# Kernel optimization log

Hardware: AMD Instinct MI355X
Metric: run time of the kernel (lower is better)

## Reference

```python
import jax, jax.numpy as jnp
import numpy as np

N_NODES = 100000
N_EDGES = 1000000
D = 128          # node_dim == out_dim (embedding_dim)
EDGE_DIM = 10
NEG_SLOPE = 0.01  # torch leaky_relu default
EPS = 1e-16       # PyG softmax denominator eps


def _leaky(x):
    return jnp.where(x >= 0, x, NEG_SLOPE * x)


def setup_inputs() -> dict:
    key = jax.random.key(0)
    ks = jax.random.split(key, 12)
    s = lambda fan_in: 1.0 / np.sqrt(fan_in)
    return {
        "x": jax.random.normal(ks[0], (N_NODES, D), jnp.float32),
        "edge_index": jax.random.randint(ks[1], (2, N_EDGES), 0, N_NODES),
        "edge_attr": jax.random.normal(ks[2], (N_EDGES, EDGE_DIM), jnp.float32),
        # q: Linear(D, D, bias=False)
        "Wq": jax.random.uniform(ks[3], (D, D), jnp.float32, -s(D), s(D)),
        # k: Linear(EDGE_DIM, D, bias=False)
        "Wk": jax.random.uniform(ks[4], (D, EDGE_DIM), jnp.float32, -s(EDGE_DIM), s(EDGE_DIM)),
        # v: Linear(EDGE_DIM, D) with bias
        "Wv": jax.random.uniform(ks[5], (D, EDGE_DIM), jnp.float32, -s(EDGE_DIM), s(EDGE_DIM)),
        "bv": jax.random.uniform(ks[6], (D,), jnp.float32, -s(EDGE_DIM), s(EDGE_DIM)),
        # attn_score_layer: Linear(2D, D) -> ReLU -> Linear(D, 1)
        "W1": jax.random.uniform(ks[7], (D, 2 * D), jnp.float32, -s(2 * D), s(2 * D)),
        "b1": jax.random.uniform(ks[8], (D,), jnp.float32, -s(2 * D), s(2 * D)),
        "W2": jax.random.uniform(ks[9], (1, D), jnp.float32, -s(D), s(D)),
        "b2": jax.random.uniform(ks[10], (1,), jnp.float32, -s(D), s(D)),
    }


def reference(x, edge_index, edge_attr, Wq, Wk, Wv, bv, W1, b1, W2, b2):
    N = x.shape[0]
    tgt = edge_index[1]                       # destination node per edge [E]
    q = x @ Wq.T                              # [N, D] node queries
    x_i = q[tgt]                              # gather target queries [E, D]
    k = _leaky(edge_attr @ Wk.T)              # [E, D]
    v = _leaky(edge_attr @ Wv.T + bv)         # [E, D]
    h = jnp.concatenate([x_i, k], axis=-1)    # [E, 2D]
    scores = (jax.nn.relu(h @ W1.T + b1) @ W2.T + b2)[:, 0]  # [E]
    # segment softmax over edges grouped by target node (PyG softmax)
    smax = jax.ops.segment_max(scores, tgt, num_segments=N)  # [N]
    e = jnp.exp(scores - smax[tgt])
    denom = jax.ops.segment_sum(e, tgt, num_segments=N)
    attn = e / (denom[tgt] + EPS)             # [E]
    out = jax.ops.segment_sum(v * attn[:, None], tgt, num_segments=N)  # [N, D]
    return out, attn
```

## Files before the change

kernel.cpp:

```cpp
#include <hip/hip_runtime.h>
#include <stdint.h>

#define NN 100000
#define NE 1000000
#define NTILES (NE / 64)
#define NB_SCAN 391

typedef __attribute__((ext_vector_type(8))) short bf16x8;
typedef __attribute__((ext_vector_type(4))) float f32x4;

static const size_t OFF_W1K   = 0;
static const size_t OFF_WVK   = 8192;
static const size_t OFF_W1BP  = 16384;
static const size_t OFF_MTB   = 49152;
static const size_t OFF_RP    = 81920;
static const size_t OFF_CUR   = 524288;
static const size_t OFF_PART  = 1048576;
static const size_t OFF_BSUM  = 1572864;
static const size_t OFF_BSUMX = 1576960;
static const size_t OFF_CNT   = 1581056;
static const size_t OFF_PT    = 2097152;
static const size_t OFF_EVALS = 10485760;
static const size_t OFF_ATTNS = 14485760;
static const size_t OFF_EAS   = 18485760;
static const size_t OFF_SNODE = 38485760;

__device__ inline unsigned short f2bf(float f) {
    const unsigned int u = __float_as_uint(f);
    return (unsigned short)((u + 0x7fffu + ((u >> 16) & 1u)) >> 16);
}

__device__ inline unsigned int cvtpk(float lo, float hi) {
    unsigned int r;
    asm("v_cvt_pk_bf16_f32 %0, %1, %2" : "=v"(r) : "v"(lo), "v"(hi));
    return r;
}

__device__ inline float lk(float v) {
    return fmaxf(v, 0.f) + 0.01f * fminf(v, 0.f);
}

union BU { bf16x8 v; uint4 u; };

__global__ __launch_bounds__(128) void prep_kernel(
    const float* __restrict__ W1, const float* __restrict__ Wq,
    const float* __restrict__ Wk, const float* __restrict__ Wv,
    unsigned short* __restrict__ w1k, unsigned short* __restrict__ wvk,
    unsigned short* __restrict__ w1bp, unsigned short* __restrict__ mtb)
{
    const int l = blockIdx.x;
    const int i = threadIdx.x;
    float acc = 0.f;
#pragma unroll 8
    for (int j = 0; j < 128; ++j)
        acc = fmaf(W1[i * 256 + j], Wq[j * 128 + l], acc);
    mtb[i * 128 + l] = f2bf(acc);
    if (i < 32) {
        w1k[l * 32 + i] = (i < 10) ? f2bf(Wk[l * 10 + i]) : (unsigned short)0;
        wvk[l * 32 + i] = (i < 10) ? f2bf(Wv[l * 10 + i]) : (unsigned short)0;
    }
    const int m = l;
    const int j = (m & ~31) + 16 * ((m >> 2) & 1) + 4 * ((m >> 3) & 3) + (m & 3);
    w1bp[i * 128 + m] = f2bf(W1[i * 256 + 128 + j]);
}

__global__ __launch_bounds__(256) void node_score_kernel(
    const float* __restrict__ x, const unsigned short* __restrict__ mtb_g,
    const float* __restrict__ b1, unsigned short* __restrict__ s_node)
{
    __shared__ __align__(16) unsigned short mt_s[128 * 136];
    const int t = threadIdx.x;
    for (int idx = t; idx < 2048; idx += 256) {
        const uint4 v = ((const uint4*)mtb_g)[idx];
        const int row = idx >> 4, q = idx & 15;
        *(uint4*)&mt_s[row * 136 + q * 8] = v;
    }
    __syncthreads();

    const int lane = t & 63;
    const int wave = t >> 6;
    const int h    = lane >> 4;
    const int e15  = lane & 15;
    const int node = blockIdx.x * 64 + wave * 16 + e15;
    const int nc   = min(node, NN - 1);
    const int lds_base = e15 * 136 + h * 8;

    const f32x4 z4 = {0.f, 0.f, 0.f, 0.f};
    f32x4 acc[8];
#pragma unroll
    for (int g = 0; g < 8; ++g) acc[g] = z4;

#pragma unroll
    for (int s = 0; s < 4; ++s) {
        const float4 xa = *(const float4*)&x[(size_t)nc * 128 + s * 32 + h * 8];
        const float4 xb = *(const float4*)&x[(size_t)nc * 128 + s * 32 + h * 8 + 4];
        BU bx;
        bx.u.x = cvtpk(xa.x, xa.y);
        bx.u.y = cvtpk(xa.z, xa.w);
        bx.u.z = cvtpk(xb.x, xb.y);
        bx.u.w = cvtpk(xb.z, xb.w);
#pragma unroll
        for (int g = 0; g < 8; ++g) {
            const bf16x8 a = *(const bf16x8*)&mt_s[lds_base + g * (16 * 136) + s * 32];
            acc[g] = __builtin_amdgcn_mfma_f32_16x16x32_bf16(a, bx.v, acc[g], 0, 0, 0);
        }
    }

    if (node < NN) {
#pragma unroll
        for (int g = 0; g < 8; ++g) {
            const float4 bb = *(const float4*)&b1[g * 16 + h * 4];
            uint2 o2;
            o2.x = cvtpk(acc[g][0] + bb.x, acc[g][1] + bb.y);
            o2.y = cvtpk(acc[g][2] + bb.z, acc[g][3] + bb.w);
            *(uint2*)&s_node[(size_t)node * 128 + g * 16 + h * 4] = o2;
        }
    }
}

__global__ __launch_bounds__(256) void hist_kernel(
    const int* __restrict__ tgt, int* __restrict__ cnt)
{
    const int e = blockIdx.x * 256 + threadIdx.x;
    if (e < NE) atomicAdd(&cnt[tgt[e]], 1);
}

__global__ __launch_bounds__(256) void scan1_kernel(
    const int* __restrict__ cnt, int* __restrict__ part, int* __restrict__ bsum)
{
    __shared__ int s[256];
    const int t = threadIdx.x;
    const int idx = blockIdx.x * 256 + t;
    const int v = (idx < NN) ? cnt[idx] : 0;
    s[t] = v;
    __syncthreads();
    for (int off = 1; off < 256; off <<= 1) {
        const int u = (t >= off) ? s[t - off] : 0;
        __syncthreads();
        s[t] += u;
        __syncthreads();
    }
    part[idx] = s[t] - v;
    if (t == 255) bsum[blockIdx.x] = s[255];
}

__global__ __launch_bounds__(512) void scan2_kernel(
    const int* __restrict__ bsum, int* __restrict__ bsumx)
{
    __shared__ int s[512];
    const int t = threadIdx.x;
    const int v = (t < NB_SCAN) ? bsum[t] : 0;
    s[t] = v;
    __syncthreads();
    for (int off = 1; off < 512; off <<= 1) {
        const int u = (t >= off) ? s[t - off] : 0;
        __syncthreads();
        s[t] += u;
        __syncthreads();
    }
    if (t < NB_SCAN) bsumx[t] = s[t] - v;
}

__global__ __launch_bounds__(256) void scan3_kernel(
    const int* __restrict__ part, const int* __restrict__ bsumx,
    int* __restrict__ rowptr, int* __restrict__ cursor)
{
    const int idx = blockIdx.x * 256 + threadIdx.x;
    if (idx < NN) {
        const int rp = part[idx] + bsumx[idx >> 8];
        rowptr[idx] = rp;
        cursor[idx] = rp;
    }
    if (idx == 0) rowptr[NN] = NE;
}

__global__ __launch_bounds__(256) void fill_kernel(
    const int* __restrict__ tgt, int* __restrict__ cursor, int2* __restrict__ pt)
{
    const int e = blockIdx.x * 256 + threadIdx.x;
    if (e < NE) {
        const int tg = tgt[e];
        const int p  = atomicAdd(&cursor[tg], 1);
        pt[p] = make_int2(e, tg);
    }
}

__global__ __launch_bounds__(256) void edge_kernel(
    const float* __restrict__ edge_attr, const int2* __restrict__ pt,
    const unsigned short* __restrict__ w1k_g, const unsigned short* __restrict__ w1bp_g,
    const float* __restrict__ W2, const float* __restrict__ b2,
    const unsigned short* __restrict__ s_node,
    float* __restrict__ e_vals, unsigned int* __restrict__ eas)
{
    __shared__ __align__(16) unsigned short w1b_s[128 * 136];

    const int t = threadIdx.x;
    for (int idx = t; idx < 2048; idx += 256) {
        const uint4 v = ((const uint4*)w1bp_g)[idx];
        const int row = idx >> 4, q = idx & 15;
        *(uint4*)&w1b_s[row * 136 + q * 8] = v;
    }

    const int lane = t & 63;
    const int wave = t >> 6;
    const int h    = lane >> 4;
    const int e15  = lane & 15;

    bf16x8 a1[8];
#pragma unroll
    for (int f = 0; f < 8; ++f)
        a1[f] = *(const bf16x8*)&w1k_g[(f * 16 + e15) * 32 + h * 8];
    const float b2v = b2[0];

    __syncthreads();

    const int lds_base = e15 * 136 + h * 8;
    const int cstep    = gridDim.x * 64;

    int c = blockIdx.x * 64 + wave * 16 + e15;

    int2 ptc = pt[min(c, NE - 1)];
    int2 ptn = pt[min(c + cstep, NE - 1)];

    uint2 sn[8];
#pragma unroll
    for (int g = 0; g < 8; ++g)
        sn[g] = *(const uint2*)&s_node[(size_t)ptc.y * 128 + g * 16 + h * 4];

    float ea0 = 0.f, ea1 = 0.f, ea2 = 0.f, ea3 = 0.f, ea4 = 0.f;
    float ea5 = 0.f, ea6 = 0.f, ea7 = 0.f, ea8 = 0.f, ea9 = 0.f;
    {
        const float* pa = edge_attr + (size_t)ptc.x * 10;
        if (h == 0) {
            const float2 u0 = *(const float2*)(pa + 0);
            const float2 u1 = *(const float2*)(pa + 2);
            const float2 u2 = *(const float2*)(pa + 4);
            const float2 u3 = *(const float2*)(pa + 6);
            ea0 = u0.x; ea1 = u0.y; ea2 = u1.x; ea3 = u1.y;
            ea4 = u2.x; ea5 = u2.y; ea6 = u3.x; ea7 = u3.y;
        } else if (h == 1) {
            const float2 u4 = *(const float2*)(pa + 8);
            ea8 = u4.x; ea9 = u4.y;
        }
    }

    for (int tile = blockIdx.x; tile < NTILES; tile += gridDim.x, c += cstep) {
        const int2 ptn2 = pt[min(c + 2 * cstep, NE - 1)];
        uint2 sn_n[8];
#pragma unroll
        for (int g = 0; g < 8; ++g)
            sn_n[g] = *(const uint2*)&s_node[(size_t)ptn.y * 128 + g * 16 + h * 4];
        float en0 = 0.f, en1 = 0.f, en2 = 0.f, en3 = 0.f, en4 = 0.f;
        float en5 = 0.f, en6 = 0.f, en7 = 0.f, en8 = 0.f, en9 = 0.f;
        {
            const float* pa = edge_attr + (size_t)ptn.x * 10;
            if (h == 0) {
                const float2 u0 = *(const float2*)(pa + 0);
                const float2 u1 = *(const float2*)(pa + 2);
                const float2 u2 = *(const float2*)(pa + 4);
                const float2 u3 = *(const float2*)(pa + 6);
                en0 = u0.x; en1 = u0.y; en2 = u1.x; en3 = u1.y;
                en4 = u2.x; en5 = u2.y; en6 = u3.x; en7 = u3.y;
            } else if (h == 1) {
                const float2 u4 = *(const float2*)(pa + 8);
                en8 = u4.x; en9 = u4.y;
            }
        }

        bf16x8 b1 = (bf16x8){0, 0, 0, 0, 0, 0, 0, 0};
        {
            unsigned int* po = eas + (size_t)c * 5;
            if (h == 0) {
                BU bu;
                bu.u.x = cvtpk(ea0, ea1);
                bu.u.y = cvtpk(ea2, ea3);
                bu.u.z = cvtpk(ea4, ea5);
                bu.u.w = cvtpk(ea6, ea7);
                b1 = bu.v;
                po[0] = bu.u.x; po[1] = bu.u.y; po[2] = bu.u.z; po[3] = bu.u.w;
            } else if (h == 1) {
                BU bu;
                bu.u.x = cvtpk(ea8, ea9);
                bu.u.y = 0; bu.u.z = 0; bu.u.w = 0;
                b1 = bu.v;
                po[4] = bu.u.x;
            }
        }

        const f32x4 z4 = {0.f, 0.f, 0.f, 0.f};
        f32x4 acc1[8];
#pragma unroll
        for (int f = 0; f < 8; ++f)
            acc1[f] = __builtin_amdgcn_mfma_f32_16x16x32_bf16(a1[f], b1, z4, 0, 0, 0);

        bf16x8 pb[4];
#pragma unroll
        for (int s = 0; s < 4; ++s) {
            BU bu;
            bu.u.x = cvtpk(lk(acc1[2 * s][0]), lk(acc1[2 * s][1]));
            bu.u.y = cvtpk(lk(acc1[2 * s][2]), lk(acc1[2 * s][3]));
            bu.u.z = cvtpk(lk(acc1[2 * s + 1][0]), lk(acc1[2 * s + 1][1]));
            bu.u.w = cvtpk(lk(acc1[2 * s + 1][2]), lk(acc1[2 * s + 1][3]));
            pb[s] = bu.v;
        }

        float p = 0.f;
#pragma unroll
        for (int g2 = 0; g2 < 4; ++g2) {
            const int gA = 2 * g2, gB = 2 * g2 + 1;
            f32x4 accA = z4, accB = z4;
#pragma unroll
            for (int s = 0; s < 4; ++s) {
                const bf16x8 a2A = *(const bf16x8*)&w1b_s[lds_base + gA * (16 * 136) + s * 32];
                const bf16x8 a2B = *(const bf16x8*)&w1b_s[lds_base + gB * (16 * 136) + s * 32];
                accA = __builtin_amdgcn_mfma_f32_16x16x32_bf16(a2A, pb[s], accA, 0, 0, 0);
                accB = __builtin_amdgcn_mfma_f32_16x16x32_bf16(a2B, pb[s], accB, 0, 0, 0);
            }
            const float4 w2A = *(const float4*)&W2[gA * 16 + h * 4];
            const float4 w2B = *(const float4*)&W2[gB * 16 + h * 4];
            const uint2 svA = sn[gA], svB = sn[gB];
            p = fmaf(fmaxf(accA[0] + __uint_as_float(svA.x << 16), 0.f), w2A.x, p);
            p = fmaf(fmaxf(accA[1] + __uint_as_float(svA.x & 0xffff0000u), 0.f), w2A.y, p);
            p = fmaf(fmaxf(accA[2] + __uint_as_float(svA.y << 16), 0.f), w2A.z, p);
            p = fmaf(fmaxf(accA[3] + __uint_as_float(svA.y & 0xffff0000u), 0.f), w2A.w, p);
            p = fmaf(fmaxf(accB[0] + __uint_as_float(svB.x << 16), 0.f), w2B.x, p);
            p = fmaf(fmaxf(accB[1] + __uint_as_float(svB.x & 0xffff0000u), 0.f), w2B.y, p);
            p = fmaf(fmaxf(accB[2] + __uint_as_float(svB.y << 16), 0.f), w2B.z, p);
            p = fmaf(fmaxf(accB[3] + __uint_as_float(svB.y & 0xffff0000u), 0.f), w2B.w, p);
        }
        p += __shfl_xor(p, 16);
        p += __shfl_xor(p, 32);
        if (lane < 16)
            e_vals[c - e15 + lane] = __expf(p + b2v);

        ptc = ptn; ptn = ptn2;
#pragma unroll
        for (int g = 0; g < 8; ++g) sn[g] = sn_n[g];
        ea0 = en0; ea1 = en1; ea2 = en2; ea3 = en3; ea4 = en4;
        ea5 = en5; ea6 = en6; ea7 = en7; ea8 = en8; ea9 = en9;
    }
}

__global__ __launch_bounds__(256) void denom_kernel(
    const int* __restrict__ rowptr, const float* __restrict__ e_vals,
    float* __restrict__ inv_denom, float* __restrict__ out)
{
    const int n = blockIdx.x * 256 + threadIdx.x;
    if (n >= NN) return;
    const int rs = rowptr[n], re = rowptr[n + 1];
    float s = 0.f;
    for (int c = rs; c < re; ++c) s += e_vals[c];
    inv_denom[n] = 1.f / (s + 1e-16f);
    if (re > rs && (rs >> 6) != ((re - 1) >> 6)) {
        const float4 z = make_float4(0.f, 0.f, 0.f, 0.f);
        float4* po = (float4*)&out[(size_t)n * 128];
#pragma unroll 8
        for (int q = 0; q < 32; ++q) po[q] = z;
    }
}

__global__ __launch_bounds__(256) void attn_kernel(
    const int2* __restrict__ pt, const float* __restrict__ e_vals,
    const float* __restrict__ inv_denom,
    float* __restrict__ attn_s, float* __restrict__ attn_out)
{
    const int c = blockIdx.x * 256 + threadIdx.x;
    if (c >= NE) return;
    const int2 p = pt[c];
    const float a = e_vals[c] * inv_denom[p.y];
    attn_s[c] = a;
    attn_out[p.x] = a;
}

__global__ __launch_bounds__(256) void vscatter_kernel(
    const int* __restrict__ rowptr, const int2* __restrict__ pt,
    const unsigned int* __restrict__ eas, const float* __restrict__ attn_s,
    const unsigned short* __restrict__ wvk_g, const float* __restrict__ bv,
    float* __restrict__ out)
{
    __shared__ __align__(16) float w_lds[64 * 132];

    const int t    = threadIdx.x;
    const int lane = t & 63;
    const int wv   = t >> 6;
    const int h    = lane >> 4;
    const int e15  = lane & 15;
    const int base = blockIdx.x * 64;
    const int c    = base + wv * 16 + e15;
    const int el   = wv * 16 + e15;

    bf16x8 av[8];
#pragma unroll
    for (int g = 0; g < 8; ++g)
        av[g] = *(const bf16x8*)&wvk_g[(g * 16 + e15) * 32 + h * 8];

    bf16x8 be = (bf16x8){0, 0, 0, 0, 0, 0, 0, 0};
    {
        const unsigned int* pe = eas + (size_t)c * 5;
        if (h == 0) {
            BU bu;
            bu.u.x = pe[0]; bu.u.y = pe[1]; bu.u.z = pe[2]; bu.u.w = pe[3];
            be = bu.v;
        } else if (h == 1) {
            BU bu;
            bu.u.x = pe[4]; bu.u.y = 0; bu.u.z = 0; bu.u.w = 0;
            be = bu.v;
        }
    }
    const float at = attn_s[c];

    const f32x4 z4 = {0.f, 0.f, 0.f, 0.f};
#pragma unroll
    for (int g = 0; g < 8; ++g) {
        const f32x4 acc = __builtin_amdgcn_mfma_f32_16x16x32_bf16(av[g], be, z4, 0, 0, 0);
        const float4 bb = *(const float4*)&bv[g * 16 + h * 4];
        float4 w;
        w.x = at * lk(acc[0] + bb.x);
        w.y = at * lk(acc[1] + bb.y);
        w.z = at * lk(acc[2] + bb.z);
        w.w = at * lk(acc[3] + bb.w);
        *(float4*)&w_lds[el * 132 + g * 16 + h * 4] = w;
    }
    __syncthreads();

    const int n_lo = (blockIdx.x == 0) ? 0 : pt[base].y;
    const int n_hi = (blockIdx.x == (int)gridDim.x - 1) ? (NN - 1) : pt[base + 64].y;

    for (int nd = n_lo + wv; nd <= n_hi; nd += 4) {
        const int rs = rowptr[nd], re = rowptr[nd + 1];
        const int lo = max(rs, base), hi = min(re, base + 64);
        float sx = 0.f, sy = 0.f;
        for (int cc = lo; cc < hi; ++cc) {
            const float2 v = *(const float2*)&w_lds[(cc - base) * 132 + lane * 2];
            sx += v.x; sy += v.y;
        }
        float* po = &out[(size_t)nd * 128 + lane * 2];
        if (rs >= base && re <= base + 64) {
            *(float2*)po = make_float2(sx, sy);
        } else {
            atomicAdd(po, sx);
            atomicAdd(po + 1, sy);
        }
    }
}

extern "C" void kernel_launch(void* const* d_in, const int* in_sizes, int n_in,
                              void* d_out, int out_size, void* d_ws, size_t ws_size,
                              hipStream_t stream)
{
    const float* x         = (const float*)d_in[0];
    const int*   eidx      = (const int*)d_in[1];
    const float* edge_attr = (const float*)d_in[2];
    const float* Wq        = (const float*)d_in[3];
    const float* Wk        = (const float*)d_in[4];
    const float* Wv        = (const float*)d_in[5];
    const float* bv        = (const float*)d_in[6];
    const float* W1        = (const float*)d_in[7];
    const float* b1        = (const float*)d_in[8];
    const float* W2        = (const float*)d_in[9];
    const float* b2        = (const float*)d_in[10];
    const int*   tgt       = eidx + NE;

    char* ws = (char*)d_ws;
    unsigned short* w1k    = (unsigned short*)(ws + OFF_W1K);
    unsigned short* wvk    = (unsigned short*)(ws + OFF_WVK);
    unsigned short* w1bp   = (unsigned short*)(ws + OFF_W1BP);
    unsigned short* mtb    = (unsigned short*)(ws + OFF_MTB);
    int*            rowptr = (int*)(ws + OFF_RP);
    int*            cursor = (int*)(ws + OFF_CUR);
    float*          invd   = (float*)(ws + OFF_CUR);
    int*            part   = (int*)(ws + OFF_PART);
    int*            bsum   = (int*)(ws + OFF_BSUM);
    int*            bsumx  = (int*)(ws + OFF_BSUMX);
    int*            cnt    = (int*)(ws + OFF_CNT);
    int2*           pt     = (int2*)(ws + OFF_PT);
    float*          e_vals = (float*)(ws + OFF_EVALS);
    float*          attn_s = (float*)(ws + OFF_ATTNS);
    unsigned int*   eas    = (unsigned int*)(ws + OFF_EAS);
    unsigned short* s_node = (unsigned short*)(ws + OFF_SNODE);

    float* out      = (float*)d_out;
    float* attn_out = out + (size_t)NN * 128;

    hipMemsetAsync(cnt, 0, (size_t)NN * sizeof(int), stream);

    prep_kernel<<<128, 128, 0, stream>>>(W1, Wq, Wk, Wv, w1k, wvk, w1bp, mtb);
    node_score_kernel<<<(NN + 63) / 64, 256, 0, stream>>>(x, mtb, b1, s_node);
    hist_kernel<<<(NE + 255) / 256, 256, 0, stream>>>(tgt, cnt);
    scan1_kernel<<<NB_SCAN, 256, 0, stream>>>(cnt, part, bsum);
    scan2_kernel<<<1, 512, 0, stream>>>(bsum, bsumx);
    scan3_kernel<<<NB_SCAN, 256, 0, stream>>>(part, bsumx, rowptr, cursor);
    fill_kernel<<<(NE + 255) / 256, 256, 0, stream>>>(tgt, cursor, pt);
    edge_kernel<<<768, 256, 0, stream>>>(edge_attr, pt, w1k, w1bp, W2, b2,
                                         s_node, e_vals, eas);
    denom_kernel<<<(NN + 255) / 256, 256, 0, stream>>>(rowptr, e_vals, invd, out);
    attn_kernel<<<(NE + 255) / 256, 256, 0, stream>>>(pt, e_vals, invd,
                                                      attn_s, attn_out);
    vscatter_kernel<<<NTILES, 256, 0, stream>>>(rowptr, pt, eas, attn_s,
                                                wvk, bv, out);
}
```

Before: 329.0 us.

## Fuse attention normalization into vscatter and pre-swizzle weights into MFMA fragment order

Removes the separate attn_kernel and computes the normalized attention inside vscatter_kernel, writing attn_out directly. This drops one launch and the attn_s round-trip through global memory. Weight matrices are stored in MFMA fragment order so the LDS fill becomes a straight copy with no padded stride, and biases and node scores are folded into the MFMA accumulator init. The edge kernel grid also grows from 768 to 1024 blocks. The unpadded LDS layout could change bank-conflict behaviour.

```diff
diff --git a/kernel.cpp b/kernel.cpp
--- a/kernel.cpp
+++ b/kernel.cpp
@@ -21,9 +21,8 @@
 static const size_t OFF_CNT   = 1581056;
 static const size_t OFF_PT    = 2097152;
 static const size_t OFF_EVALS = 10485760;
-static const size_t OFF_ATTNS = 14485760;
-static const size_t OFF_EAS   = 18485760;
-static const size_t OFF_SNODE = 38485760;
+static const size_t OFF_EAS   = 14485760;
+static const size_t OFF_SNODE = 34485760;
 
 __device__ inline unsigned short f2bf(float f) {
     const unsigned int u = __float_as_uint(f);
@@ -38,6 +37,12 @@
 
 __device__ inline float lk(float v) {
     return fmaxf(v, 0.f) + 0.01f * fminf(v, 0.f);
+}
+
+__device__ __host__ inline int mfma_order(int i, int m) {
+    const int g = i >> 4, e15 = i & 15;
+    const int s = m >> 5, h = (m >> 3) & 3, jj = m & 7;
+    return (g * 4 + s) * 512 + (e15 * 4 + h) * 8 + jj;
 }
 
 union BU { bf16x8 v; uint4 u; };
@@ -54,27 +59,24 @@
 #pragma unroll 8
     for (int j = 0; j < 128; ++j)
         acc = fmaf(W1[i * 256 + j], Wq[j * 128 + l], acc);
-    mtb[i * 128 + l] = f2bf(acc);
+    mtb[mfma_order(i, l)] = f2bf(acc);
     if (i < 32) {
         w1k[l * 32 + i] = (i < 10) ? f2bf(Wk[l * 10 + i]) : (unsigned short)0;
         wvk[l * 32 + i] = (i < 10) ? f2bf(Wv[l * 10 + i]) : (unsigned short)0;
     }
     const int m = l;
     const int j = (m & ~31) + 16 * ((m >> 2) & 1) + 4 * ((m >> 3) & 3) + (m & 3);
-    w1bp[i * 128 + m] = f2bf(W1[i * 256 + 128 + j]);
+    w1bp[mfma_order(i, m)] = f2bf(W1[i * 256 + 128 + j]);
 }
 
 __global__ __launch_bounds__(256) void node_score_kernel(
     const float* __restrict__ x, const unsigned short* __restrict__ mtb_g,
     const float* __restrict__ b1, unsigned short* __restrict__ s_node)
 {
-    __shared__ __align__(16) unsigned short mt_s[128 * 136];
+    __shared__ __align__(16) unsigned short mt_s[128 * 128];
     const int t = threadIdx.x;
-    for (int idx = t; idx < 2048; idx += 256) {
-        const uint4 v = ((const uint4*)mtb_g)[idx];
-        const int row = idx >> 4, q = idx & 15;
-        *(uint4*)&mt_s[row * 136 + q * 8] = v;
-    }
+    for (int idx = t; idx < 2048; idx += 256)
+        *(uint4*)&mt_s[idx * 8] = ((const uint4*)mtb_g)[idx];
     __syncthreads();
 
     const int lane = t & 63;
@@ -83,12 +85,14 @@
     const int e15  = lane & 15;
     const int node = blockIdx.x * 64 + wave * 16 + e15;
     const int nc   = min(node, NN - 1);
-    const int lds_base = e15 * 136 + h * 8;
-
-    const f32x4 z4 = {0.f, 0.f, 0.f, 0.f};
+    const int slot8 = (e15 * 4 + h) * 8;
+
     f32x4 acc[8];
 #pragma unroll
-    for (int g = 0; g < 8; ++g) acc[g] = z4;
+    for (int g = 0; g < 8; ++g) {
+        const float4 bb = *(const float4*)&b1[g * 16 + h * 4];
+        acc[g][0] = bb.x; acc[g][1] = bb.y; acc[g][2] = bb.z; acc[g][3] = bb.w;
+    }
 
 #pragma unroll
     for (int s = 0; s < 4; ++s) {
@@ -101,7 +105,7 @@
         bx.u.w = cvtpk(xb.z, xb.w);
 #pragma unroll
         for (int g = 0; g < 8; ++g) {
-            const bf16x8 a = *(const bf16x8*)&mt_s[lds_base + g * (16 * 136) + s * 32];
+            const bf16x8 a = *(const bf16x8*)&mt_s[(g * 4 + s) * 512 + slot8];
             acc[g] = __builtin_amdgcn_mfma_f32_16x16x32_bf16(a, bx.v, acc[g], 0, 0, 0);
         }
     }
@@ -109,10 +113,9 @@
     if (node < NN) {
 #pragma unroll
         for (int g = 0; g < 8; ++g) {
-            const float4 bb = *(const float4*)&b1[g * 16 + h * 4];
             uint2 o2;
-            o2.x = cvtpk(acc[g][0] + bb.x, acc[g][1] + bb.y);
-            o2.y = cvtpk(acc[g][2] + bb.z, acc[g][3] + bb.w);
+            o2.x = cvtpk(acc[g][0], acc[g][1]);
+            o2.y = cvtpk(acc[g][2], acc[g][3]);
             *(uint2*)&s_node[(size_t)node * 128 + g * 16 + h * 4] = o2;
         }
     }
@@ -192,14 +195,11 @@
     const unsigned short* __restrict__ s_node,
     float* __restrict__ e_vals, unsigned int* __restrict__ eas)
 {
-    __shared__ __align__(16) unsigned short w1b_s[128 * 136];
+    __shared__ __align__(16) unsigned short w1b_s[128 * 128];
 
     const int t = threadIdx.x;
-    for (int idx = t; idx < 2048; idx += 256) {
-        const uint4 v = ((const uint4*)w1bp_g)[idx];
-        const int row = idx >> 4, q = idx & 15;
-        *(uint4*)&w1b_s[row * 136 + q * 8] = v;
-    }
+    for (int idx = t; idx < 2048; idx += 256)
+        *(uint4*)&w1b_s[idx * 8] = ((const uint4*)w1bp_g)[idx];
 
     const int lane = t & 63;
     const int wave = t >> 6;
@@ -214,8 +214,8 @@
 
     __syncthreads();
 
-    const int lds_base = e15 * 136 + h * 8;
-    const int cstep    = gridDim.x * 64;
+    const int slot8 = (e15 * 4 + h) * 8;
+    const int cstep = gridDim.x * 64;
 
     int c = blockIdx.x * 64 + wave * 16 + e15;
 
@@ -308,25 +308,33 @@
 #pragma unroll
         for (int g2 = 0; g2 < 4; ++g2) {
             const int gA = 2 * g2, gB = 2 * g2 + 1;
-            f32x4 accA = z4, accB = z4;
+            const uint2 svA = sn[gA], svB = sn[gB];
+            f32x4 accA, accB;
+            accA[0] = __uint_as_float(svA.x << 16);
+            accA[1] = __uint_as_float(svA.x & 0xffff0000u);
+            accA[2] = __uint_as_float(svA.y << 16);
+            accA[3] = __uint_as_float(svA.y & 0xffff0000u);
+            accB[0] = __uint_as_float(svB.x << 16);
+            accB[1] = __uint_as_float(svB.x & 0xffff0000u);
+            accB[2] = __uint_as_float(svB.y << 16);
+            accB[3] = __uint_as_float(svB.y & 0xffff0000u);
 #pragma unroll
             for (int s = 0; s < 4; ++s) {
-                const bf16x8 a2A = *(const bf16x8*)&w1b_s[lds_base + gA * (16 * 136) + s * 32];
-                const bf16x8 a2B = *(const bf16x8*)&w1b_s[lds_base + gB * (16 * 136) + s * 32];
+                const bf16x8 a2A = *(const bf16x8*)&w1b_s[(gA * 4 + s) * 512 + slot8];
+                const bf16x8 a2B = *(const bf16x8*)&w1b_s[(gB * 4 + s) * 512 + slot8];
                 accA = __builtin_amdgcn_mfma_f32_16x16x32_bf16(a2A, pb[s], accA, 0, 0, 0);
                 accB = __builtin_amdgcn_mfma_f32_16x16x32_bf16(a2B, pb[s], accB, 0, 0, 0);
             }
             const float4 w2A = *(const float4*)&W2[gA * 16 + h * 4];
             const float4 w2B = *(const float4*)&W2[gB * 16 + h * 4];
-            const uint2 svA = sn[gA], svB = sn[gB];
-            p = fmaf(fmaxf(accA[0] + __uint_as_float(svA.x << 16), 0.f), w2A.x, p);
-            p = fmaf(fmaxf(accA[1] + __uint_as_float(svA.x & 0xffff0000u), 0.f), w2A.y, p);
-            p = fmaf(fmaxf(accA[2] + __uint_as_float(svA.y << 16), 0.f), w2A.z, p);
-            p = fmaf(fmaxf(accA[3] + __uint_as_float(svA.y & 0xffff0000u), 0.f), w2A.w, p);
-            p = fmaf(fmaxf(accB[0] + __uint_as_float(svB.x << 16), 0.f), w2B.x, p);
-            p = fmaf(fmaxf(accB[1] + __uint_as_float(svB.x & 0xffff0000u), 0.f), w2B.y, p);
-            p = fmaf(fmaxf(accB[2] + __uint_as_float(svB.y << 16), 0.f), w2B.z, p);
-            p = fmaf(fmaxf(accB[3] + __uint_as_float(svB.y & 0xffff0000u), 0.f), w2B.w, p);
+            p = fmaf(fmaxf(accA[0], 0.f), w2A.x, p);
+            p = fmaf(fmaxf(accA[1], 0.f), w2A.y, p);
+            p = fmaf(fmaxf(accA[2], 0.f), w2A.z, p);
+            p = fmaf(fmaxf(accA[3], 0.f), w2A.w, p);
+            p = fmaf(fmaxf(accB[0], 0.f), w2B.x, p);
+            p = fmaf(fmaxf(accB[1], 0.f), w2B.y, p);
+            p = fmaf(fmaxf(accB[2], 0.f), w2B.z, p);
+            p = fmaf(fmaxf(accB[3], 0.f), w2B.w, p);
         }
         p += __shfl_xor(p, 16);
         p += __shfl_xor(p, 32);
@@ -359,24 +367,12 @@
     }
 }
 
-__global__ __launch_bounds__(256) void attn_kernel(
-    const int2* __restrict__ pt, const float* __restrict__ e_vals,
-    const float* __restrict__ inv_denom,
-    float* __restrict__ attn_s, float* __restrict__ attn_out)
-{
-    const int c = blockIdx.x * 256 + threadIdx.x;
-    if (c >= NE) return;
-    const int2 p = pt[c];
-    const float a = e_vals[c] * inv_denom[p.y];
-    attn_s[c] = a;
-    attn_out[p.x] = a;
-}
-
 __global__ __launch_bounds__(256) void vscatter_kernel(
     const int* __restrict__ rowptr, const int2* __restrict__ pt,
-    const unsigned int* __restrict__ eas, const float* __restrict__ attn_s,
+    const unsigned int* __restrict__ eas, const float* __restrict__ e_vals,
+    const float* __restrict__ inv_denom,
     const unsigned short* __restrict__ wvk_g, const float* __restrict__ bv,
-    float* __restrict__ out)
+    float* __restrict__ out, float* __restrict__ attn_out)
 {
     __shared__ __align__(16) float w_lds[64 * 132];
 
@@ -393,6 +389,10 @@
 #pragma unroll
     for (int g = 0; g < 8; ++g)
         av[g] = *(const bf16x8*)&wvk_g[(g * 16 + e15) * 32 + h * 8];
+
+    const int2 pc = pt[c];
+    const float at = e_vals[c] * inv_denom[pc.y];
+    attn_out[pc.x] = at;
 
     bf16x8 be = (bf16x8){0, 0, 0, 0, 0, 0, 0, 0};
     {
@@ -407,18 +407,18 @@
             be = bu.v;
         }
     }
-    const float at = attn_s[c];
-
-    const f32x4 z4 = {0.f, 0.f, 0.f, 0.f};
+
 #pragma unroll
     for (int g = 0; g < 8; ++g) {
-        const f32x4 acc = __builtin_amdgcn_mfma_f32_16x16x32_bf16(av[g], be, z4, 0, 0, 0);
         const float4 bb = *(const float4*)&bv[g * 16 + h * 4];
+        f32x4 cb;
+        cb[0] = bb.x; cb[1] = bb.y; cb[2] = bb.z; cb[3] = bb.w;
+        const f32x4 acc = __builtin_amdgcn_mfma_f32_16x16x32_bf16(av[g], be, cb, 0, 0, 0);
         float4 w;
-        w.x = at * lk(acc[0] + bb.x);
-        w.y = at * lk(acc[1] + bb.y);
-        w.z = at * lk(acc[2] + bb.z);
-        w.w = at * lk(acc[3] + bb.w);
+        w.x = at * lk(acc[0]);
+        w.y = at * lk(acc[1]);
+        w.z = at * lk(acc[2]);
+        w.w = at * lk(acc[3]);
         *(float4*)&w_lds[el * 132 + g * 16 + h * 4] = w;
     }
     __syncthreads();
@@ -475,7 +475,6 @@
     int*            cnt    = (int*)(ws + OFF_CNT);
     int2*           pt     = (int2*)(ws + OFF_PT);
     float*          e_vals = (float*)(ws + OFF_EVALS);
-    float*          attn_s = (float*)(ws + OFF_ATTNS);
     unsigned int*   eas    = (unsigned int*)(ws + OFF_EAS);
     unsigned short* s_node = (unsigned short*)(ws + OFF_SNODE);
 
@@ -491,11 +490,9 @@
     scan2_kernel<<<1, 512, 0, stream>>>(bsum, bsumx);
     scan3_kernel<<<NB_SCAN, 256, 0, stream>>>(part, bsumx, rowptr, cursor);
     fill_kernel<<<(NE + 255) / 256, 256, 0, stream>>>(tgt, cursor, pt);
-    edge_kernel<<<768, 256, 0, stream>>>(edge_attr, pt, w1k, w1bp, W2, b2,
-                                         s_node, e_vals, eas);
+    edge_kernel<<<1024, 256, 0, stream>>>(edge_attr, pt, w1k, w1bp, W2, b2,
+                                          s_node, e_vals, eas);
     denom_kernel<<<(NN + 255) / 256, 256, 0, stream>>>(rowptr, e_vals, invd, out);
-    attn_kernel<<<(NE + 255) / 256, 256, 0, stream>>>(pt, e_vals, invd,
-                                                      attn_s, attn_out);
-    vscatter_kernel<<<NTILES, 256, 0, stream>>>(rowptr, pt, eas, attn_s,
-                                                wvk, bv, out);
-}
+    vscatter_kernel<<<NTILES, 256, 0, stream>>>(rowptr, pt, eas, e_vals, invd,
+                                                wvk, bv, out, attn_out);
+}
```

Measured after the change: 320.7 us. 2.5% less time.

## Fuse attention normalization into vscatter with persistent grid-stride tiles

Applied to the files above, without the earlier changes.

Removes the separate attn_kernel and computes attn = e_vals * inv_denom inside vscatter, writing attn_out directly and dropping the attn_s intermediate buffer. vscatter becomes a persistent kernel with 1024 blocks looping over tiles, so the Wv fragments and bias are loaded once per block, and the bias is folded into the MFMA accumulator input. This saves one launch and a round trip of a 1M-float array. The cost is extra __syncthreads per tile and fewer blocks in flight to hide latency.

```diff
diff --git a/kernel.cpp b/kernel.cpp
--- a/kernel.cpp
+++ b/kernel.cpp
@@ -21,9 +21,8 @@
 static const size_t OFF_CNT   = 1581056;
 static const size_t OFF_PT    = 2097152;
 static const size_t OFF_EVALS = 10485760;
-static const size_t OFF_ATTNS = 14485760;
-static const size_t OFF_EAS   = 18485760;
-static const size_t OFF_SNODE = 38485760;
+static const size_t OFF_EAS   = 14485760;
+static const size_t OFF_SNODE = 34485760;
 
 __device__ inline unsigned short f2bf(float f) {
     const unsigned int u = __float_as_uint(f);
@@ -359,24 +358,12 @@
     }
 }
 
-__global__ __launch_bounds__(256) void attn_kernel(
-    const int2* __restrict__ pt, const float* __restrict__ e_vals,
-    const float* __restrict__ inv_denom,
-    float* __restrict__ attn_s, float* __restrict__ attn_out)
-{
-    const int c = blockIdx.x * 256 + threadIdx.x;
-    if (c >= NE) return;
-    const int2 p = pt[c];
-    const float a = e_vals[c] * inv_denom[p.y];
-    attn_s[c] = a;
-    attn_out[p.x] = a;
-}
-
 __global__ __launch_bounds__(256) void vscatter_kernel(
     const int* __restrict__ rowptr, const int2* __restrict__ pt,
-    const unsigned int* __restrict__ eas, const float* __restrict__ attn_s,
+    const unsigned int* __restrict__ eas, const float* __restrict__ e_vals,
+    const float* __restrict__ inv_denom,
     const unsigned short* __restrict__ wvk_g, const float* __restrict__ bv,
-    float* __restrict__ out)
+    float* __restrict__ out, float* __restrict__ attn_out)
 {
     __shared__ __align__(16) float w_lds[64 * 132];
 
@@ -385,61 +372,71 @@
     const int wv   = t >> 6;
     const int h    = lane >> 4;
     const int e15  = lane & 15;
-    const int base = blockIdx.x * 64;
-    const int c    = base + wv * 16 + e15;
     const int el   = wv * 16 + e15;
 
     bf16x8 av[8];
-#pragma unroll
-    for (int g = 0; g < 8; ++g)
+    float4 bb[8];
+#pragma unroll
+    for (int g = 0; g < 8; ++g) {
         av[g] = *(const bf16x8*)&wvk_g[(g * 16 + e15) * 32 + h * 8];
-
-    bf16x8 be = (bf16x8){0, 0, 0, 0, 0, 0, 0, 0};
-    {
-        const unsigned int* pe = eas + (size_t)c * 5;
-        if (h == 0) {
-            BU bu;
-            bu.u.x = pe[0]; bu.u.y = pe[1]; bu.u.z = pe[2]; bu.u.w = pe[3];
-            be = bu.v;
-        } else if (h == 1) {
-            BU bu;
-            bu.u.x = pe[4]; bu.u.y = 0; bu.u.z = 0; bu.u.w = 0;
-            be = bu.v;
-        }
-    }
-    const float at = attn_s[c];
-
-    const f32x4 z4 = {0.f, 0.f, 0.f, 0.f};
-#pragma unroll
-    for (int g = 0; g < 8; ++g) {
-        const f32x4 acc = __builtin_amdgcn_mfma_f32_16x16x32_bf16(av[g], be, z4, 0, 0, 0);
-        const float4 bb = *(const float4*)&bv[g * 16 + h * 4];
-        float4 w;
-        w.x = at * lk(acc[0] + bb.x);
-        w.y = at * lk(acc[1] + bb.y);
-        w.z = at * lk(acc[2] + bb.z);
-        w.w = at * lk(acc[3] + bb.w);
-        *(float4*)&w_lds[el * 132 + g * 16 + h * 4] = w;
-    }
-    __syncthreads();
-
-    const int n_lo = (blockIdx.x == 0) ? 0 : pt[base].y;
-    const int n_hi = (blockIdx.x == (int)gridDim.x - 1) ? (NN - 1) : pt[base + 64].y;
-
-    for (int nd = n_lo + wv; nd <= n_hi; nd += 4) {
-        const int rs = rowptr[nd], re = rowptr[nd + 1];
-        const int lo = max(rs, base), hi = min(re, base + 64);
-        float sx = 0.f, sy = 0.f;
-        for (int cc = lo; cc < hi; ++cc) {
-            const float2 v = *(const float2*)&w_lds[(cc - base) * 132 + lane * 2];
-            sx += v.x; sy += v.y;
-        }
-        float* po = &out[(size_t)nd * 128 + lane * 2];
-        if (rs >= base && re <= base + 64) {
-            *(float2*)po = make_float2(sx, sy);
-        } else {
-            atomicAdd(po, sx);
-            atomicAdd(po + 1, sy);
+        bb[g] = *(const float4*)&bv[g * 16 + h * 4];
+    }
+
+    for (int tile = blockIdx.x; tile < NTILES; tile += gridDim.x) {
+        const int base = tile * 64;
+        const int c    = base + el;
+
+        const int2 pc = pt[c];
+        const float at = e_vals[c] * inv_denom[pc.y];
+        if (h == 0) attn_out[pc.x] = at;
+
+        bf16x8 be = (bf16x8){0, 0, 0, 0, 0, 0, 0, 0};
+        {
+            const unsigned int* pe = eas + (size_t)c * 5;
+            if (h == 0) {
+                BU bu;
+                bu.u.x = pe[0]; bu.u.y = pe[1]; bu.u.z = pe[2]; bu.u.w = pe[3];
+                be = bu.v;
+            } else if (h == 1) {
+                BU bu;
+                bu.u.x = pe[4]; bu.u.y = 0; bu.u.z = 0; bu.u.w = 0;
+                be = bu.v;
+            }
+        }
+
+        __syncthreads();
+#pragma unroll
+        for (int g = 0; g < 8; ++g) {
+            f32x4 cb;
+            cb[0] = bb[g].x; cb[1] = bb[g].y; cb[2] = bb[g].z; cb[3] = bb[g].w;
+            const f32x4 acc = __builtin_amdgcn_mfma_f32_16x16x32_bf16(av[g], be, cb, 0, 0, 0);
+            float4 w;
+            w.x = at * lk(acc[0]);
+            w.y = at * lk(acc[1]);
+            w.z = at * lk(acc[2]);
+            w.w = at * lk(acc[3]);
+            *(float4*)&w_lds[el * 132 + g * 16 + h * 4] = w;
+        }
+        __syncthreads();
+
+        const int n_lo = (tile == 0) ? 0 : pt[base].y;
+        const int n_hi = (tile == NTILES - 1) ? (NN - 1) : pt[base + 64].y;
+
+        for (int nd = n_lo + wv; nd <= n_hi; nd += 4) {
+            const int rs = rowptr[nd], re = rowptr[nd + 1];
+            const int lo = max(rs, base), hi = min(re, base + 64);
+            float sx = 0.f, sy = 0.f;
+            for (int cc = lo; cc < hi; ++cc) {
+                const float2 v = *(const float2*)&w_lds[(cc - base) * 132 + lane * 2];
+                sx += v.x; sy += v.y;
+            }
+            float* po = &out[(size_t)nd * 128 + lane * 2];
+            if (rs >= base && re <= base + 64) {
+                *(float2*)po = make_float2(sx, sy);
+            } else {
+                atomicAdd(po, sx);
+                atomicAdd(po + 1, sy);
+            }
         }
     }
 }
@@ -475,7 +472,6 @@
     int*            cnt    = (int*)(ws + OFF_CNT);
     int2*           pt     = (int2*)(ws + OFF_PT);
     float*          e_vals = (float*)(ws + OFF_EVALS);
-    float*          attn_s = (float*)(ws + OFF_ATTNS);
     unsigned int*   eas    = (unsigned int*)(ws + OFF_EAS);
     unsigned short* s_node = (unsigned short*)(ws + OFF_SNODE);
 
@@ -494,8 +490,6 @@
     edge_kernel<<<768, 256, 0, stream>>>(edge_attr, pt, w1k, w1bp, W2, b2,
                                          s_node, e_vals, eas);
     denom_kernel<<<(NN + 255) / 256, 256, 0, stream>>>(rowptr, e_vals, invd, out);
-    attn_kernel<<<(NE + 255) / 256, 256, 0, stream>>>(pt, e_vals, invd,
-                                                      attn_s, attn_out);
-    vscatter_kernel<<<NTILES, 256, 0, stream>>>(rowptr, pt, eas, attn_s,
-                                                wvk, bv, out);
-}
+    vscatter_kernel<<<1024, 256, 0, stream>>>(rowptr, pt, eas, e_vals, invd,
+                                              wvk, bv, out, attn_out);
+}
```

After: 306.0 us. 7.0% less time.
